# Optimization experiments

Measured on AMD Instinct MI355X. Metric: run time of the kernel, lower is better.

The kernel has to match this reference:

```python
import jax, jax.numpy as jnp
import numpy as np

EPS = 1e-4

def _conv(x, W):
    # x: [B,H,W,Cin], W: [3,3,Cin,Cout] -> SAME submanifold-style dense conv
    return jax.lax.conv_general_dilated(x, W, (1, 1), 'SAME',
                                        dimension_numbers=('NHWC', 'HWIO', 'NHWC'))

def _bn_relu(x, m, g, b):
    # BatchNormReLU over active sites only (scn semantics)
    mm = m[..., None]
    n = jnp.maximum(mm.sum(), 1.0)
    mean = (x * mm).sum((0, 1, 2)) / n
    var = (((x - mean) ** 2) * mm).sum((0, 1, 2)) / n
    y = (x - mean) * jax.lax.rsqrt(var + EPS) * g + b
    return jnp.maximum(y, 0.0) * mm

def _maxpool(x, m):
    # scn.MaxPooling(2, 3, 2): 3x3 window, stride 2, VALID; output active if any input active
    neg = jnp.where(m[..., None] > 0, x, -1e30)
    p = jax.lax.reduce_window(neg, -1e30, jax.lax.max, (1, 3, 3, 1), (1, 2, 2, 1), 'VALID')
    m2 = jax.lax.reduce_window(m, 0.0, jax.lax.max, (1, 3, 3), (1, 2, 2), 'VALID')
    return jnp.where(m2[..., None] > 0, p, 0.0), m2


def setup_inputs() -> dict:
    key = jax.random.key(0)
    ks = jax.random.split(key, 16)
    B, H, W = 2048, 23, 31
    x = jax.random.normal(ks[0], (B, H, W, 2), dtype=jnp.float32)
    mask = jax.random.randint(ks[1], (B, H, W), 0, 2, dtype=jnp.int32)
    def w(k, shape, s=0.05):
        return jax.random.normal(k, shape, dtype=jnp.float32) * s
    params = {
        'x': x, 'mask': mask,
        'W1': w(ks[2], (3, 3, 2, 16)),   'g1': jnp.ones(16),  'b1': jnp.zeros(16),
        'W2': w(ks[3], (3, 3, 16, 32)),  'g2': jnp.ones(32),  'b2': jnp.zeros(32),
        'W3': w(ks[4], (3, 3, 32, 64)),  'g3': jnp.ones(64),  'b3': jnp.zeros(64),
        'W4': w(ks[5], (3, 3, 64, 128)), 'g4': jnp.ones(128), 'b4': jnp.zeros(128),
        'Wl': w(ks[6], (3, 3, 128, 4 * 256)), 'bl': jnp.zeros(4 * 256),
        'lw1': w(ks[7], (8960, 1024), 0.02), 'lb1': jnp.zeros(1024),
        'lw2': w(ks[8], (1024, 5 * 7 * 12), 0.02), 'lb2': jnp.zeros(5 * 7 * 12),
    }
    return params


def reference(x, mask, W1, g1, b1, W2, g2, b2, W3, g3, b3, W4, g4, b4,
              Wl, bl, lw1, lb1, lw2, lb2):
    m = mask.astype(x.dtype)
    xm = x * m[..., None]
    h = _bn_relu(_conv(xm, W1) * m[..., None], m, g1, b1)
    h = _bn_relu(_conv(h, W2) * m[..., None], m, g2, b2)
    h, m = _maxpool(h, m)                          # [B,11,15,32]
    h = _bn_relu(_conv(h, W3) * m[..., None], m, g3, b3)
    h = _bn_relu(_conv(h, W4) * m[..., None], m, g4, b4)
    h, m = _maxpool(h, m)                          # [B,5,7,128]
    # sparse ConvLSTM, single step, zero initial hidden/cell state
    gates = (_conv(h, Wl) + bl) * m[..., None]     # [B,5,7,1024]
    i, f, o, g_ = jnp.split(gates, 4, axis=-1)
    c = jax.nn.sigmoid(i) * jnp.tanh(g_)
    hh = jax.nn.sigmoid(o) * jnp.tanh(c) * m[..., None]  # [B,5,7,256]
    # SparseToDense gives [B,C,H,W]; flatten in (C,H,W) order like torch .view
    flat = jnp.transpose(hh, (0, 3, 1, 2)).reshape(hh.shape[0], -1)  # [B,8960]
    y = jnp.maximum(flat @ lw1 + lb1, 0.0)
    y = y @ lw2 + lb2
    return y.reshape(-1, 5, 7, 12)
```

## Files before the change

### kernel.cpp

```cpp
#include <hip/hip_runtime.h>
#include <hip/hip_bf16.h>
#include <math.h>

using bf16 = __hip_bfloat16;

typedef short s8v __attribute__((ext_vector_type(8)));
typedef float f4v __attribute__((ext_vector_type(4)));

static constexpr int  BB  = 2048;
static constexpr int  IH  = 23, IW = 31;
static constexpr int  PH  = 11, PW = 15;
static constexpr int  QH  = 5,  QW = 7;
static constexpr long NSITE1 = (long)BB * IH * IW;
static constexpr long NSITE2 = (long)BB * PH * PW;
static constexpr long NSITE3 = (long)BB * QH * QW;

static constexpr long OFF_S1 = 0,   OFF_Q1 = 64;
static constexpr long OFF_S2 = 128, OFF_Q2 = 192;
static constexpr long OFF_S3 = 256, OFF_Q3 = 320;
static constexpr long OFF_S4 = 384, OFF_Q4 = 512;
static constexpr long OFF_N1 = 640, OFF_N2 = 641;
static constexpr long OFF_SC1 = 704,  OFF_SH1 = 768;
static constexpr long OFF_SC2 = 832,  OFF_SH2 = 896;
static constexpr long OFF_SC3 = 960,  OFF_SH3 = 1024;
static constexpr long OFF_SC4 = 1088, OFF_SH4 = 1216;
static constexpr long OFF_M0 = 2048;
static constexpr long OFF_M1 = OFF_M0 + NSITE1;
static constexpr long OFF_M2 = OFF_M1 + NSITE2;
static constexpr long OFF_BF = 1871872;
static constexpr long SZ_A   = 43253760L;
static constexpr long WB2_A  = 25000000L;
static constexpr long WB3_B  = 22000000L;
static constexpr long WB4_B  = 22100000L;
static constexpr long WBL_A  = 20000000L;
static constexpr long WFC1_B = 23000000L;
static constexpr long WFC2_B = 33000000L;
static constexpr long BKT_A  = 40000000L;
static constexpr long BKT_B  = 35000000L;

__device__ __forceinline__ float b2f(bf16 v) { return __bfloat162float(v); }
__device__ __forceinline__ bf16  f2b(float v) { return __float2bfloat16(v); }
__device__ __forceinline__ float sigmoidf_(float x) {
    return __builtin_amdgcn_rcpf(1.f + __expf(-x));
}
__device__ __forceinline__ float tanhf_(float x) {
    float xc = fminf(fmaxf(x, -15.f), 15.f);
    float t = __expf(-2.f * xc);
    return (1.f - t) * __builtin_amdgcn_rcpf(1.f + t);
}

__device__ __forceinline__ void ld8(const bf16* p, float* f) {
    union { uint4 u; unsigned short s[8]; } cv;
    cv.u = *(const uint4*)p;
#pragma unroll
    for (int i = 0; i < 8; i++) f[i] = __uint_as_float(((unsigned int)cv.s[i]) << 16);
}
__device__ __forceinline__ void st8(bf16* p, const float* f) {
    union { uint4 u; bf16 h[8]; } cv;
#pragma unroll
    for (int i = 0; i < 8; i++) cv.h[i] = f2b(f[i]);
    *(uint4*)p = cv.u;
}

__global__ void cvt_w_k(const float* __restrict__ W, bf16* __restrict__ wb,
                        int CIN, int CINP, int COUT, int total) {
    int idx = blockIdx.x * 256 + threadIdx.x;
    if (idx >= total) return;
    int ci  = idx % CINP;
    int t2  = idx / CINP;
    int co  = t2 % COUT;
    int tap = t2 / COUT;
    wb[idx] = (ci < CIN) ? f2b(W[((long)(tap * CIN + ci)) * COUT + co]) : f2b(0.f);
}

__global__ void cvt_wl3_k(const float* __restrict__ Wl, bf16* __restrict__ wbl3) {
    int idx = blockIdx.x * 256 + threadIdx.x;
    if (idx >= 884736) return;
    int kidx = idx & 31;
    int n    = (idx >> 5) % 768;
    int kk   = (idx >> 5) / 768 % 4;
    int tap  = idx / (32 * 768 * 4);
    int g = n >> 8, c = n & 255;
    int col = (g == 0) ? c : (g == 1 ? 512 + c : 768 + c);
    int cin = kk * 32 + kidx;
    wbl3[idx] = f2b(Wl[((long)(tap * 128 + cin)) * 1024 + col]);
}

__global__ void cvt_fc1T8_k(const float* __restrict__ lw1, bf16* __restrict__ wfc1) {
    int t = blockIdx.x * 256 + threadIdx.x;
    if (t >= 1146880) return;
    int j   = t & 1023;
    int k8g = t >> 10;
    int hw  = k8g >> 5;
    int c8  = k8g & 31;
    float f[8];
#pragma unroll
    for (int c7 = 0; c7 < 8; c7++)
        f[c7] = lw1[((long)((c8 * 8 + c7) * 35 + hw)) * 1024 + j];
    st8(wfc1 + (long)t * 8, f);
}

__global__ void cvt_fc2T8_k(const float* __restrict__ lw2, bf16* __restrict__ whi,
                            bf16* __restrict__ wlo) {
    int t = blockIdx.x * 256 + threadIdx.x;
    if (t >= 57344) return;
    int n  = t % 448;
    int k8 = t / 448;
    union { uint4 u; bf16 h8[8]; } h, l;
#pragma unroll
    for (int ki = 0; ki < 8; ki++) {
        float v = (n < 420) ? lw2[(long)(k8 * 8 + ki) * 420 + n] : 0.f;
        bf16 hb = f2b(v);
        h.h8[ki] = hb;
        l.h8[ki] = f2b(v - b2f(hb));
    }
    *(uint4*)(whi + (long)t * 8) = h.u;
    *(uint4*)(wlo + (long)t * 8) = l.u;
}

__global__ void prep_k(const float* __restrict__ x, const int* __restrict__ mask,
                       float* __restrict__ m0, bf16* __restrict__ xm) {
    long idx = (long)blockIdx.x * 256 + threadIdx.x;
    if (idx >= NSITE1) return;
    float m = (mask[idx] != 0) ? 1.f : 0.f;
    m0[idx] = m;
    xm[idx * 2 + 0] = f2b(x[idx * 2 + 0] * m);
    xm[idx * 2 + 1] = f2b(x[idx * 2 + 1] * m);
}

__global__ void conv1_k(const bf16* __restrict__ xm, const float* __restrict__ Wt,
                        const float* __restrict__ m0, bf16* __restrict__ out,
                        float* __restrict__ bkt, float* __restrict__ cnt) {
    __shared__ float s_s[16], s_q[16], s_c;
    const int H = IH, W = IW;
    int tid = threadIdx.x;
    int L = tid & 63;
    if (tid < 16) { s_s[tid] = 0.f; s_q[tid] = 0.f; }
    if (tid == 0) s_c = 0.f;
    __syncthreads();
    long site = (long)blockIdx.x * 256 + tid;
    float acc[16];
#pragma unroll
    for (int i = 0; i < 16; i++) acc[i] = 0.f;
    float mk = 0.f;
    if (site < NSITE1) {
        mk = m0[site];
        if (mk > 0.f) {
            int w = (int)(site % W); int h = (int)((site / W) % H);
            for (int tap = 0; tap < 9; tap++) {
                int dh = tap / 3 - 1, dw = tap % 3 - 1;
                int nh = h + dh, nw = w + dw;
                if (nh < 0 || nh >= H || nw < 0 || nw >= W) continue;
                long ns = site + (long)dh * W + dw;
                float i0 = b2f(xm[ns * 2 + 0]), i1 = b2f(xm[ns * 2 + 1]);
                const float* wp = Wt + tap * 32;
#pragma unroll
                for (int co = 0; co < 16; co++) acc[co] += i0 * wp[co] + i1 * wp[16 + co];
            }
        }
        st8(out + site * 16, acc);
        st8(out + site * 16 + 8, acc + 8);
    }
#pragma unroll
    for (int i = 0; i < 16; i++) {
        float vb = (site < NSITE1) ? b2f(f2b(acc[i])) : 0.f;
        float s = vb, q2 = vb * vb;
#pragma unroll
        for (int off = 32; off > 0; off >>= 1) {
            s  += __shfl_xor(s, off);
            q2 += __shfl_xor(q2, off);
        }
        if (L == 0) { atomicAdd(&s_s[i], s); atomicAdd(&s_q[i], q2); }
    }
    {
        float c = (mk > 0.f) ? 1.f : 0.f;
#pragma unroll
        for (int off = 32; off > 0; off >>= 1) c += __shfl_xor(c, off);
        if (L == 0) atomicAdd(&s_c, c);
    }
    __syncthreads();
    int bk = blockIdx.x & 63;
    if (tid < 16) {
        atomicAdd(bkt + (long)bk * 32 + tid, s_s[tid]);
        atomicAdd(bkt + (long)bk * 32 + 16 + tid, s_q[tid]);
    }
    if (tid == 0) atomicAdd(cnt, s_c);
}

template<int CIN, int CINP, int COUT, int KK, int MT_W, int NT_W, int H, int W,
         bool ZPAD, bool BN, bool STATS, bool CNT>
__global__ void conv_mfma(const bf16* __restrict__ in, const bf16* __restrict__ wb,
                          const float* __restrict__ mask,
                          const float* __restrict__ scale, const float* __restrict__ shift,
                          bf16* __restrict__ out,
                          float* __restrict__ bkt, float* __restrict__ cnt) {
    constexpr int NT   = COUT / 16;
    constexpr int NWN  = NT / NT_W;
    constexpr int HALO = W + 1;
    constexpr int REG  = 64 + 2 * HALO;
    constexpr int SE   = CIN + 8;
    constexpr int CHPS = CIN / 8;
    __shared__ bf16 smem[(REG + 1) * SE];
    __shared__ float s_s[COUT], s_q[COUT], s_c;

    const int tid = threadIdx.x;
    const int wv = tid >> 6;
    const int L  = tid & 63;
    const int q  = (L >> 4);
    const int lm = L & 15;
    const int wn = wv % NWN;
    const int wm = wv / NWN;
    const int mt0 = wm * MT_W;
    const long base = (long)blockIdx.x * 64;
    const long nsites = (long)gridDim.x * 64;

    for (int c = tid; c < REG * CHPS; c += 256) {
        int s = c / CHPS;
        int o = c % CHPS;
        long gs = base - HALO + s;
        uint4 v = {0u, 0u, 0u, 0u};
        if (gs >= 0 && gs < nsites) {
            v = *(const uint4*)(in + gs * CIN + o * 8);
            if (BN) {
                float mk = mask[gs];
                union { uint4 u; unsigned short us[8]; } cv; cv.u = v;
                union { uint4 u; bf16 h[8]; } ov;
#pragma unroll
                for (int i = 0; i < 8; i++) {
                    float f = __uint_as_float(((unsigned int)cv.us[i]) << 16);
                    int ch = o * 8 + i;
                    float r = fmaxf(f * scale[ch] + shift[ch], 0.f);
                    ov.h[i] = f2b(mk > 0.f ? r : 0.f);
                }
                v = ov.u;
            }
        }
        *(uint4*)(smem + s * SE + o * 8) = v;
    }
    if (ZPAD) {
        uint4 z = {0u, 0u, 0u, 0u};
        for (int s = tid; s < REG; s += 256)
            *(uint4*)(smem + s * SE + CIN) = z;
        if (tid == 0)
            *(uint4*)(smem + REG * SE) = z;
    }
    if (STATS) {
        if (tid < COUT) { s_s[tid] = 0.f; s_q[tid] = 0.f; }
        if (tid == 0) s_c = 0.f;
    }
    __syncthreads();

    int hh[MT_W], ww[MT_W];
#pragma unroll
    for (int i = 0; i < MT_W; i++) {
        long s = base + (mt0 + i) * 16 + lm;
        ww[i] = (int)(s % W);
        hh[i] = (int)((s / W) % H);
    }
    const int lbase = mt0 * 16 + lm + HALO;

    f4v acc[MT_W][NT_W];
#pragma unroll
    for (int i = 0; i < MT_W; i++)
#pragma unroll
        for (int j = 0; j < NT_W; j++) acc[i][j] = (f4v){0.f, 0.f, 0.f, 0.f};

    for (int tap = 0; tap < 9; tap++) {
        const int dh = tap / 3 - 1, dw = tap % 3 - 1;
        const int dlo = dh * W + dw;
#pragma unroll
        for (int kk = 0; kk < KK; kk++) {
            s8v a[MT_W];
#pragma unroll
            for (int i = 0; i < MT_W; i++) {
                int nh = hh[i] + dh, nw = ww[i] + dw;
                bool ok = (nh >= 0) & (nh < H) & (nw < W) & (nw >= 0);
                s8v t = *(const s8v*)(smem + (lbase + i * 16 + dlo) * SE + kk * 32 + q * 8);
                a[i] = ok ? t : (s8v){0, 0, 0, 0, 0, 0, 0, 0};
            }
#pragma unroll
            for (int j = 0; j < NT_W; j++) {
                int co = (wn * NT_W + j) * 16 + lm;
                s8v b = *(const s8v*)(wb + ((long)(tap * COUT + co)) * CINP + kk * 32 + q * 8);
#pragma unroll
                for (int i = 0; i < MT_W; i++)
                    acc[i][j] = __builtin_amdgcn_mfma_f32_16x16x32_bf16(a[i], b, acc[i][j], 0, 0, 0);
            }
        }
    }

    float ls[NT_W], lq[NT_W];
#pragma unroll
    for (int j = 0; j < NT_W; j++) { ls[j] = 0.f; lq[j] = 0.f; }
    float lc = 0.f;
#pragma unroll
    for (int i = 0; i < MT_W; i++) {
#pragma unroll
        for (int r = 0; r < 4; r++) {
            long so = base + (mt0 + i) * 16 + q * 4 + r;
            float mk = mask[so];
            if (CNT) { if (wv == 0 && lm == 0) lc += (mk > 0.f) ? 1.f : 0.f; }
#pragma unroll
            for (int j = 0; j < NT_W; j++) {
                int co = (wn * NT_W + j) * 16 + lm;
                bf16 ob = f2b(mk > 0.f ? acc[i][j][r] : 0.f);
                out[so * COUT + co] = ob;
                if (STATS) { float vb = b2f(ob); ls[j] += vb; lq[j] += vb * vb; }
            }
        }
    }
    if (STATS) {
#pragma unroll
        for (int j = 0; j < NT_W; j++) {
            ls[j] += __shfl_xor(ls[j], 16);
            ls[j] += __shfl_xor(ls[j], 32);
            lq[j] += __shfl_xor(lq[j], 16);
            lq[j] += __shfl_xor(lq[j], 32);
            if (q == 0) {
                int co = (wn * NT_W + j) * 16 + lm;
                atomicAdd(&s_s[co], ls[j]);
                atomicAdd(&s_q[co], lq[j]);
            }
        }
        if (CNT) {
            lc += __shfl_xor(lc, 16);
            lc += __shfl_xor(lc, 32);
            if (wv == 0 && L == 0) atomicAdd(&s_c, lc);
        }
        __syncthreads();
        int bk = blockIdx.x & 63;
        if (tid < COUT) {
            atomicAdd(bkt + (long)bk * 2 * COUT + tid, s_s[tid]);
            atomicAdd(bkt + (long)bk * 2 * COUT + COUT + tid, s_q[tid]);
        }
        if (CNT && tid == 0) atomicAdd(cnt, s_c);
    }
}

template<int C>
__global__ void bn_param_bkt(const float* __restrict__ bkt, const float* __restrict__ count,
                             const float* __restrict__ g, const float* __restrict__ b,
                             float* __restrict__ scale, float* __restrict__ shift) {
    int c = threadIdx.x;
    if (c >= C) return;
    float s = 0.f, q2 = 0.f;
    for (int k = 0; k < 64; k++) {
        s  += bkt[(long)k * 2 * C + c];
        q2 += bkt[(long)k * 2 * C + C + c];
    }
    float n = fmaxf(count[0], 1.f);
    float mean = s / n;
    float var  = q2 / n - mean * mean;
    float sc = (1.f / sqrtf(var + 1e-4f)) * g[c];
    scale[c] = sc;
    shift[c] = b[c] - mean * sc;
}

template<int C>
__global__ void maxpool_bn(const bf16* __restrict__ in, const float* __restrict__ min_,
                           const float* __restrict__ scale, const float* __restrict__ shift,
                           bf16* __restrict__ out, float* __restrict__ mout,
                           int B, int H, int W, int OH, int OW) {
    long i8 = (long)blockIdx.x * 256 + threadIdx.x;
    long total8 = (long)B * OH * OW * C / 8;
    if (i8 >= total8) return;
    long e0 = i8 * 8;
    int c0 = (int)(e0 % C);
    long osite = e0 / C;
    int ow = (int)(osite % OW); long t2 = osite / OW; int oh = (int)(t2 % OH); long b = t2 / OH;
    float sc[8], sh[8];
#pragma unroll
    for (int i = 0; i < 8; i++) { sc[i] = scale[c0 + i]; sh[i] = shift[c0 + i]; }
    float mm = 0.f, p[8];
#pragma unroll
    for (int i = 0; i < 8; i++) p[i] = -1e30f;
    for (int kh = 0; kh < 3; kh++)
    for (int kw = 0; kw < 3; kw++) {
        int h = oh * 2 + kh, w = ow * 2 + kw;
        long is = ((long)b * H + h) * W + w;
        float mv = min_[is];
        if (mv > 0.f) {
            mm = 1.f;
            float f[8];
            ld8(in + is * C + c0, f);
#pragma unroll
            for (int i = 0; i < 8; i++) p[i] = fmaxf(p[i], f[i] * sc[i] + sh[i]);
        }
    }
    float o[8];
#pragma unroll
    for (int i = 0; i < 8; i++) o[i] = (mm > 0.f) ? fmaxf(p[i], 0.f) : 0.f;
    st8(out + e0, o);
    if (c0 == 0) mout[osite] = mm;
}

__global__ void maxpool_p2t(const bf16* __restrict__ c4, const float* __restrict__ m1,
                            const float* __restrict__ scale, const float* __restrict__ shift,
                            bf16* __restrict__ p2T8, float* __restrict__ m2h) {
    int t = blockIdx.x * 256 + threadIdx.x;
    if (t >= 1146880) return;
    int b  = t & 2047;
    int q2 = t >> 11;
    int hw = q2 % 35;
    int k8 = q2 / 35;
    int oh = hw / QW, ow = hw % QW;
    int c0 = k8 * 8;
    float sc[8], sh[8];
#pragma unroll
    for (int i = 0; i < 8; i++) { sc[i] = scale[c0 + i]; sh[i] = shift[c0 + i]; }
    float mm = 0.f, p[8];
#pragma unroll
    for (int i = 0; i < 8; i++) p[i] = -1e30f;
    for (int kh = 0; kh < 3; kh++)
    for (int kw = 0; kw < 3; kw++) {
        int h = oh * 2 + kh, w = ow * 2 + kw;
        long is = ((long)b * PH + h) * PW + w;
        float mv = m1[is];
        if (mv > 0.f) {
            mm = 1.f;
            float f[8];
            ld8(c4 + is * 128 + c0, f);
#pragma unroll
            for (int i = 0; i < 8; i++) p[i] = fmaxf(p[i], f[i] * sc[i] + sh[i]);
        }
    }
    float o[8];
#pragma unroll
    for (int i = 0; i < 8; i++) o[i] = (mm > 0.f) ? fmaxf(p[i], 0.f) : 0.f;
    st8(p2T8 + (long)t * 8, o);
    if (k8 == 0) m2h[hw * 2048 + b] = mm;
}

__global__ void __launch_bounds__(256, 3)
gates_mfma(const bf16* __restrict__ p2T8, const bf16* __restrict__ wbl3,
           const float* __restrict__ bl, const float* __restrict__ m2h,
           bf16* __restrict__ goutT8) {
    __shared__ bf16 abuf[16 * 64 * 8];
    __shared__ bf16 sm[64][136];
    const int bi = blockIdx.x;
    const int half = bi & 1;
    const int g2 = bi >> 1;
    const int hw = g2 >> 5;
    const int b0 = (g2 & 31) * 64;
    const int h = hw / QW, w = hw % QW;
    const int tid = threadIdx.x;
    const int wv = tid >> 6;
    const int L  = tid & 63;
    const int q  = L >> 4;
    const int lm = L & 15;

    f4v acc[4][2][3];
#pragma unroll
    for (int i = 0; i < 4; i++)
#pragma unroll
        for (int j = 0; j < 2; j++)
#pragma unroll
            for (int g = 0; g < 3; g++) acc[i][j][g] = (f4v){0.f, 0.f, 0.f, 0.f};

    for (int tap = 0; tap < 9; tap++) {
        const int dh = tap / 3 - 1, dw = tap % 3 - 1;
        const int nh = h + dh, nw = w + dw;
        if (nh < 0 || nh >= QH || nw < 0 || nw >= QW) continue;
        const int hwn = hw + dh * QW + dw;

        __syncthreads();
        for (int c = tid; c < 1024; c += 256) {
            int kq = c >> 6;
            int bb = c & 63;
            uint4 v = *(const uint4*)(p2T8 + (((long)(kq * 35 + hwn)) * 2048 + b0 + bb) * 8);
            *(uint4*)(abuf + (long)c * 8) = v;
        }
        __syncthreads();

#pragma unroll
        for (int kk = 0; kk < 4; kk++) {
            s8v a[4];
#pragma unroll
            for (int i = 0; i < 4; i++)
                a[i] = *(const s8v*)(abuf + (((kk * 4 + q) * 64) + i * 16 + lm) * 8);
            const bf16* slab = wbl3 + ((long)(tap * 4 + kk)) * 768 * 32 + (long)q * 8;
#pragma unroll
            for (int j = 0; j < 2; j++) {
                int cc = half * 8 + wv * 2 + j;
#pragma unroll
                for (int g = 0; g < 3; g++) {
                    int n = g * 256 + cc * 16 + lm;
                    s8v b = *(const s8v*)(slab + (long)n * 32);
#pragma unroll
                    for (int i = 0; i < 4; i++)
                        acc[i][j][g] = __builtin_amdgcn_mfma_f32_16x16x32_bf16(a[i], b, acc[i][j][g], 0, 0, 0);
                }
            }
        }
    }
#pragma unroll
    for (int j = 0; j < 2; j++) {
        int cc = half * 8 + wv * 2 + j;
        int c = cc * 16 + lm;
        int cl = (wv * 2 + j) * 16 + lm;
        float bi_ = bl[c], bo_ = bl[512 + c], bg_ = bl[768 + c];
#pragma unroll
        for (int i = 0; i < 4; i++) {
#pragma unroll
            for (int r = 0; r < 4; r++) {
                int b_in = i * 16 + q * 4 + r;
                float m = m2h[hw * 2048 + b0 + b_in];
                float val = 0.f;
                if (m > 0.f) {
                    float iv = acc[i][j][0][r] + bi_;
                    float ov = acc[i][j][1][r] + bo_;
                    float gv = acc[i][j][2][r] + bg_;
                    float ct = sigmoidf_(iv) * tanhf_(gv);
                    val = sigmoidf_(ov) * tanhf_(ct);
                }
                sm[b_in][cl] = f2b(val);
            }
        }
    }
    __syncthreads();
#pragma unroll
    for (int k = 0; k < 4; k++) {
        int e = k * 256 + tid;
        int c8l = e >> 6, b_in = e & 63;
        union { uint4 u; bf16 h8[8]; } v;
#pragma unroll
        for (int i = 0; i < 8; i++) v.h8[i] = sm[b_in][c8l * 8 + i];
        long dst = ((long)(hw * 32 + half * 16 + c8l)) * 2048 + b0 + b_in;
        *(uint4*)(goutT8 + dst * 8) = v.u;
    }
}

__global__ void fc1_mfma(const bf16* __restrict__ AT8, const bf16* __restrict__ WT8,
                         const float* __restrict__ lb1, bf16* __restrict__ y1) {
    const int tid = threadIdx.x;
    const int wv = tid >> 6;
    const int L  = tid & 63;
    const int q  = L >> 4, lm = L & 15;
    const int wm = wv >> 1, wn = wv & 1;
    const int bm = blockIdx.x & 31;
    const int bn = blockIdx.x >> 5;
    const int m0 = bm * 64 + wm * 32;
    const int n0 = bn * 64 + wn * 32;

    f4v acc[2][2];
#pragma unroll
    for (int i = 0; i < 2; i++)
#pragma unroll
        for (int j = 0; j < 2; j++) acc[i][j] = (f4v){0.f, 0.f, 0.f, 0.f};

#pragma unroll 2
    for (int k8 = 0; k8 < 1120; k8 += 4) {
        long ar = ((long)(k8 + q)) * 2048;
        long br = ((long)(k8 + q)) * 1024;
        s8v a0 = *(const s8v*)(AT8 + (ar + m0 + lm) * 8);
        s8v a1 = *(const s8v*)(AT8 + (ar + m0 + 16 + lm) * 8);
        s8v b0 = *(const s8v*)(WT8 + (br + n0 + lm) * 8);
        s8v b1 = *(const s8v*)(WT8 + (br + n0 + 16 + lm) * 8);
        acc[0][0] = __builtin_amdgcn_mfma_f32_16x16x32_bf16(a0, b0, acc[0][0], 0, 0, 0);
        acc[0][1] = __builtin_amdgcn_mfma_f32_16x16x32_bf16(a0, b1, acc[0][1], 0, 0, 0);
        acc[1][0] = __builtin_amdgcn_mfma_f32_16x16x32_bf16(a1, b0, acc[1][0], 0, 0, 0);
        acc[1][1] = __builtin_amdgcn_mfma_f32_16x16x32_bf16(a1, b1, acc[1][1], 0, 0, 0);
    }
#pragma unroll
    for (int i = 0; i < 2; i++) {
#pragma unroll
        for (int j = 0; j < 2; j++) {
            int nn = n0 + j * 16 + lm;
            float bias = lb1[nn];
#pragma unroll
            for (int r = 0; r < 4; r++) {
                int mm = m0 + i * 16 + q * 4 + r;
                y1[(long)mm * 1024 + nn] = f2b(fmaxf(acc[i][j][r] + bias, 0.f));
            }
        }
    }
}

__global__ void fc2_mfma(const bf16* __restrict__ y1, const bf16* __restrict__ whi,
                         const bf16* __restrict__ wlo, const float* __restrict__ lb2,
                         float* __restrict__ out) {
    const int tid = threadIdx.x;
    const int wv = tid >> 6;
    const int L  = tid & 63;
    const int q  = L >> 4, lm = L & 15;
    const int wm = wv >> 1, wn = wv & 1;
    const int bm = blockIdx.x % 32;
    const int bn = blockIdx.x / 32;
    const int m0 = bm * 64 + wm * 32;
    const int n0 = bn * 64 + wn * 32;

    f4v acc[2][2];
#pragma unroll
    for (int i = 0; i < 2; i++)
#pragma unroll
        for (int j = 0; j < 2; j++) acc[i][j] = (f4v){0.f, 0.f, 0.f, 0.f};

#pragma unroll 2
    for (int k8 = 0; k8 < 128; k8 += 4) {
        const bf16* arow = y1 + (long)(k8 + q) * 8;
        long br = ((long)(k8 + q)) * 448;
        s8v a0 = *(const s8v*)(arow + (long)(m0 + lm) * 1024);
        s8v a1 = *(const s8v*)(arow + (long)(m0 + 16 + lm) * 1024);
        s8v h0 = *(const s8v*)(whi + (br + n0 + lm) * 8);
        s8v h1 = *(const s8v*)(whi + (br + n0 + 16 + lm) * 8);
        s8v l0 = *(const s8v*)(wlo + (br + n0 + lm) * 8);
        s8v l1 = *(const s8v*)(wlo + (br + n0 + 16 + lm) * 8);
        acc[0][0] = __builtin_amdgcn_mfma_f32_16x16x32_bf16(a0, h0, acc[0][0], 0, 0, 0);
        acc[0][1] = __builtin_amdgcn_mfma_f32_16x16x32_bf16(a0, h1, acc[0][1], 0, 0, 0);
        acc[1][0] = __builtin_amdgcn_mfma_f32_16x16x32_bf16(a1, h0, acc[1][0], 0, 0, 0);
        acc[1][1] = __builtin_amdgcn_mfma_f32_16x16x32_bf16(a1, h1, acc[1][1], 0, 0, 0);
        acc[0][0] = __builtin_amdgcn_mfma_f32_16x16x32_bf16(a0, l0, acc[0][0], 0, 0, 0);
        acc[0][1] = __builtin_amdgcn_mfma_f32_16x16x32_bf16(a0, l1, acc[0][1], 0, 0, 0);
        acc[1][0] = __builtin_amdgcn_mfma_f32_16x16x32_bf16(a1, l0, acc[1][0], 0, 0, 0);
        acc[1][1] = __builtin_amdgcn_mfma_f32_16x16x32_bf16(a1, l1, acc[1][1], 0, 0, 0);
    }
#pragma unroll
    for (int j = 0; j < 2; j++) {
        int nn = n0 + j * 16 + lm;
        if (nn >= 420) continue;
        float bias = lb2[nn];
#pragma unroll
        for (int i = 0; i < 2; i++) {
#pragma unroll
            for (int r = 0; r < 4; r++) {
                int mm = m0 + i * 16 + q * 4 + r;
                out[(long)mm * 420 + nn] = acc[i][j][r] + bias;
            }
        }
    }
}

extern "C" void kernel_launch(void* const* d_in, const int* in_sizes, int n_in,
                              void* d_out, int out_size, void* d_ws, size_t ws_size,
                              hipStream_t stream) {
    const float* x    = (const float*)d_in[0];
    const int*   mask = (const int*)d_in[1];
    const float* W1 = (const float*)d_in[2];
    const float* g1 = (const float*)d_in[3];
    const float* b1 = (const float*)d_in[4];
    const float* W2 = (const float*)d_in[5];
    const float* g2 = (const float*)d_in[6];
    const float* b2 = (const float*)d_in[7];
    const float* W3 = (const float*)d_in[8];
    const float* g3 = (const float*)d_in[9];
    const float* b3 = (const float*)d_in[10];
    const float* W4 = (const float*)d_in[11];
    const float* g4 = (const float*)d_in[12];
    const float* b4 = (const float*)d_in[13];
    const float* Wl = (const float*)d_in[14];
    const float* bl = (const float*)d_in[15];
    const float* lw1 = (const float*)d_in[16];
    const float* lb1 = (const float*)d_in[17];
    const float* lw2 = (const float*)d_in[18];
    const float* lb2 = (const float*)d_in[19];
    float* out = (float*)d_out;

    float* ws = (float*)d_ws;
    float* m0 = ws + OFF_M0;
    float* m1 = ws + OFF_M1;
    float* m2h = ws + OFF_M2;
    bf16* bufA = (bf16*)(ws + OFF_BF);
    bf16* bufB = bufA + SZ_A;

    bf16* c1     = bufA;
    bf16* xm     = bufB;
    bf16* c2     = bufB;
    bf16* p1     = bufA;
    bf16* c3     = bufB;
    bf16* c4     = bufA;
    bf16* p2T8   = bufB;
    bf16* goutT8 = bufA;
    bf16* y1     = bufB;
    bf16* wb2    = bufA + WB2_A;
    bf16* wb3    = bufB + WB3_B;
    bf16* wb4    = bufB + WB4_B;
    bf16* wbl3   = bufA + WBL_A;
    bf16* wfc1   = bufB + WFC1_B;
    bf16* wfc2h  = bufB + WFC2_B;
    bf16* wfc2l  = wfc2h + 458752;

    float* bkt16  = (float*)(bufA + BKT_A);
    float* bkt32  = bkt16 + 2048;
    float* bkt64  = bkt32 + 4096;
    float* bkt128 = (float*)(bufB + BKT_B);

    hipMemsetAsync(ws, 0, 4096, stream);
    hipMemsetAsync(bkt16, 0, (2048 + 4096 + 8192) * 4, stream);

    prep_k<<<(int)((NSITE1 + 255) / 256), 256, 0, stream>>>(x, mask, m0, xm);
    cvt_w_k<<<(9216 + 255) / 256, 256, 0, stream>>>(W2, wb2, 16, 32, 32, 9216);

    conv1_k<<<(int)((NSITE1 + 255) / 256), 256, 0, stream>>>(xm, W1, m0, c1, bkt16, ws + OFF_N1);
    bn_param_bkt<16><<<1, 16, 0, stream>>>(bkt16, ws + OFF_N1, g1, b1, ws + OFF_SC1, ws + OFF_SH1);

    conv_mfma<16, 32, 32, 1, 2, 1, IH, IW, true, true, true, false>
        <<<(int)(NSITE1 / 64), 256, 0, stream>>>(c1, wb2, m0, ws + OFF_SC1, ws + OFF_SH1, c2,
                                                 bkt32, nullptr);
    bn_param_bkt<32><<<1, 32, 0, stream>>>(bkt32, ws + OFF_N1, g2, b2, ws + OFF_SC2, ws + OFF_SH2);

    maxpool_bn<32><<<(int)(NSITE2 * 32 / 8 / 256), 256, 0, stream>>>(c2, m0, ws + OFF_SC2, ws + OFF_SH2,
                                                                     p1, m1, BB, IH, IW, PH, PW);

    hipMemsetAsync(bkt128, 0, 16384 * 4, stream);
    cvt_w_k<<<(18432 + 255) / 256, 256, 0, stream>>>(W3, wb3, 32, 32, 64, 18432);
    cvt_w_k<<<(73728 + 255) / 256, 256, 0, stream>>>(W4, wb4, 64, 64, 128, 73728);
    cvt_fc1T8_k<<<(1146880 + 255) / 256, 256, 0, stream>>>(lw1, wfc1);
    cvt_fc2T8_k<<<(57344 + 255) / 256, 256, 0, stream>>>(lw2, wfc2h, wfc2l);

    conv_mfma<32, 32, 64, 1, 4, 1, PH, PW, false, false, true, true>
        <<<(int)(NSITE2 / 64), 256, 0, stream>>>(p1, wb3, m1, ws + OFF_SC2, ws + OFF_SH2, c3,
                                                 bkt64, ws + OFF_N2);
    bn_param_bkt<64><<<1, 64, 0, stream>>>(bkt64, ws + OFF_N2, g3, b3, ws + OFF_SC3, ws + OFF_SH3);

    conv_mfma<64, 64, 128, 2, 4, 2, PH, PW, false, true, true, false>
        <<<(int)(NSITE2 / 64), 256, 0, stream>>>(c3, wb4, m1, ws + OFF_SC3, ws + OFF_SH3, c4,
                                                 bkt128, nullptr);
    bn_param_bkt<128><<<1, 128, 0, stream>>>(bkt128, ws + OFF_N2, g4, b4, ws + OFF_SC4, ws + OFF_SH4);

    maxpool_p2t<<<(1146880 + 255) / 256, 256, 0, stream>>>(c4, m1, ws + OFF_SC4, ws + OFF_SH4, p2T8, m2h);

    cvt_wl3_k<<<(884736 + 255) / 256, 256, 0, stream>>>(Wl, wbl3);

    gates_mfma<<<2240, 256, 0, stream>>>(p2T8, wbl3, bl, m2h, goutT8);

    fc1_mfma<<<512, 256, 0, stream>>>(goutT8, wfc1, lb1, y1);

    fc2_mfma<<<224, 256, 0, stream>>>(y1, wfc2h, wfc2l, lb2, out);
}
```

Baseline: 891.6 us.

## Fold BN parameter kernels into consumers and merge weight-conversion launches

Removes the four single-block bn_param_bkt launches by having each consumer kernel (conv_mfma with BN, maxpool_bn, maxpool_p2t) reduce the 64 stat buckets into shared-memory scale/shift at block start. It also merges prep with the W2 conversion and the W3/W4/fc1/fc2 weight conversions into single multi-role kernels, and consolidates memsets. This cuts launch count and serial gaps between tiny kernels. In exchange every block redundantly sums the buckets and adds a barrier before its main work.

```diff
diff --git a/kernel.cpp b/kernel.cpp
--- a/kernel.cpp
+++ b/kernel.cpp
@@ -15,15 +15,7 @@
 static constexpr long NSITE2 = (long)BB * PH * PW;
 static constexpr long NSITE3 = (long)BB * QH * QW;
 
-static constexpr long OFF_S1 = 0,   OFF_Q1 = 64;
-static constexpr long OFF_S2 = 128, OFF_Q2 = 192;
-static constexpr long OFF_S3 = 256, OFF_Q3 = 320;
-static constexpr long OFF_S4 = 384, OFF_Q4 = 512;
 static constexpr long OFF_N1 = 640, OFF_N2 = 641;
-static constexpr long OFF_SC1 = 704,  OFF_SH1 = 768;
-static constexpr long OFF_SC2 = 832,  OFF_SH2 = 896;
-static constexpr long OFF_SC3 = 960,  OFF_SH3 = 1024;
-static constexpr long OFF_SC4 = 1088, OFF_SH4 = 1216;
 static constexpr long OFF_M0 = 2048;
 static constexpr long OFF_M1 = OFF_M0 + NSITE1;
 static constexpr long OFF_M2 = OFF_M1 + NSITE2;
@@ -36,7 +28,7 @@
 static constexpr long WFC1_B = 23000000L;
 static constexpr long WFC2_B = 33000000L;
 static constexpr long BKT_A  = 40000000L;
-static constexpr long BKT_B  = 35000000L;
+static constexpr long BKT_B  = 34000000L;
 
 __device__ __forceinline__ float b2f(bf16 v) { return __bfloat162float(v); }
 __device__ __forceinline__ bf16  f2b(float v) { return __float2bfloat16(v); }
@@ -62,9 +54,8 @@
     *(uint4*)p = cv.u;
 }
 
-__global__ void cvt_w_k(const float* __restrict__ W, bf16* __restrict__ wb,
-                        int CIN, int CINP, int COUT, int total) {
-    int idx = blockIdx.x * 256 + threadIdx.x;
+__device__ __forceinline__ void cvt_w_body(const float* __restrict__ W, bf16* __restrict__ wb,
+                                           int CIN, int CINP, int COUT, int total, int idx) {
     if (idx >= total) return;
     int ci  = idx % CINP;
     int t2  = idx / CINP;
@@ -73,59 +64,57 @@
     wb[idx] = (ci < CIN) ? f2b(W[((long)(tap * CIN + ci)) * COUT + co]) : f2b(0.f);
 }
 
-__global__ void cvt_wl3_k(const float* __restrict__ Wl, bf16* __restrict__ wbl3) {
-    int idx = blockIdx.x * 256 + threadIdx.x;
-    if (idx >= 884736) return;
-    int kidx = idx & 31;
-    int n    = (idx >> 5) % 768;
-    int kk   = (idx >> 5) / 768 % 4;
-    int tap  = idx / (32 * 768 * 4);
-    int g = n >> 8, c = n & 255;
-    int col = (g == 0) ? c : (g == 1 ? 512 + c : 768 + c);
-    int cin = kk * 32 + kidx;
-    wbl3[idx] = f2b(Wl[((long)(tap * 128 + cin)) * 1024 + col]);
-}
-
-__global__ void cvt_fc1T8_k(const float* __restrict__ lw1, bf16* __restrict__ wfc1) {
-    int t = blockIdx.x * 256 + threadIdx.x;
-    if (t >= 1146880) return;
-    int j   = t & 1023;
-    int k8g = t >> 10;
-    int hw  = k8g >> 5;
-    int c8  = k8g & 31;
-    float f[8];
-#pragma unroll
-    for (int c7 = 0; c7 < 8; c7++)
-        f[c7] = lw1[((long)((c8 * 8 + c7) * 35 + hw)) * 1024 + j];
-    st8(wfc1 + (long)t * 8, f);
-}
-
-__global__ void cvt_fc2T8_k(const float* __restrict__ lw2, bf16* __restrict__ whi,
-                            bf16* __restrict__ wlo) {
-    int t = blockIdx.x * 256 + threadIdx.x;
-    if (t >= 57344) return;
-    int n  = t % 448;
-    int k8 = t / 448;
-    union { uint4 u; bf16 h8[8]; } h, l;
-#pragma unroll
-    for (int ki = 0; ki < 8; ki++) {
-        float v = (n < 420) ? lw2[(long)(k8 * 8 + ki) * 420 + n] : 0.f;
-        bf16 hb = f2b(v);
-        h.h8[ki] = hb;
-        l.h8[ki] = f2b(v - b2f(hb));
-    }
-    *(uint4*)(whi + (long)t * 8) = h.u;
-    *(uint4*)(wlo + (long)t * 8) = l.u;
-}
-
-__global__ void prep_k(const float* __restrict__ x, const int* __restrict__ mask,
-                       float* __restrict__ m0, bf16* __restrict__ xm) {
-    long idx = (long)blockIdx.x * 256 + threadIdx.x;
-    if (idx >= NSITE1) return;
-    float m = (mask[idx] != 0) ? 1.f : 0.f;
-    m0[idx] = m;
-    xm[idx * 2 + 0] = f2b(x[idx * 2 + 0] * m);
-    xm[idx * 2 + 1] = f2b(x[idx * 2 + 1] * m);
+__global__ void prep_cvtw2_k(const float* __restrict__ x, const int* __restrict__ mask,
+                             float* __restrict__ m0, bf16* __restrict__ xm,
+                             const float* __restrict__ W2, bf16* __restrict__ wb2) {
+    int bid = blockIdx.x, tid = threadIdx.x;
+    if (bid < 5704) {
+        long idx = (long)bid * 256 + tid;
+        float m = (mask[idx] != 0) ? 1.f : 0.f;
+        m0[idx] = m;
+        xm[idx * 2 + 0] = f2b(x[idx * 2 + 0] * m);
+        xm[idx * 2 + 1] = f2b(x[idx * 2 + 1] * m);
+    } else {
+        cvt_w_body(W2, wb2, 16, 32, 32, 9216, (bid - 5704) * 256 + tid);
+    }
+}
+
+__global__ void cvt_all_k(const float* __restrict__ W3, const float* __restrict__ W4,
+                          const float* __restrict__ lw1, const float* __restrict__ lw2,
+                          bf16* __restrict__ wb3, bf16* __restrict__ wb4,
+                          bf16* __restrict__ wfc1, bf16* __restrict__ whi,
+                          bf16* __restrict__ wlo) {
+    int bid = blockIdx.x, tid = threadIdx.x;
+    if (bid < 72) {
+        cvt_w_body(W3, wb3, 32, 32, 64, 18432, bid * 256 + tid);
+    } else if (bid < 360) {
+        cvt_w_body(W4, wb4, 64, 64, 128, 73728, (bid - 72) * 256 + tid);
+    } else if (bid < 4840) {
+        int t = (bid - 360) * 256 + tid;
+        int j   = t & 1023;
+        int k8g = t >> 10;
+        int hw  = k8g >> 5;
+        int c8  = k8g & 31;
+        float f[8];
+#pragma unroll
+        for (int c7 = 0; c7 < 8; c7++)
+            f[c7] = lw1[((long)((c8 * 8 + c7) * 35 + hw)) * 1024 + j];
+        st8(wfc1 + (long)t * 8, f);
+    } else {
+        int t = (bid - 4840) * 256 + tid;
+        int n  = t % 448;
+        int k8 = t / 448;
+        union { uint4 u; bf16 h8[8]; } h, l;
+#pragma unroll
+        for (int ki = 0; ki < 8; ki++) {
+            float v = (n < 420) ? lw2[(long)(k8 * 8 + ki) * 420 + n] : 0.f;
+            bf16 hb = f2b(v);
+            h.h8[ki] = hb;
+            l.h8[ki] = f2b(v - b2f(hb));
+        }
+        *(uint4*)(whi + (long)t * 8) = h.u;
+        *(uint4*)(wlo + (long)t * 8) = l.u;
+    }
 }
 
 __global__ void conv1_k(const bf16* __restrict__ xm, const float* __restrict__ Wt,
@@ -191,9 +180,10 @@
          bool ZPAD, bool BN, bool STATS, bool CNT>
 __global__ void conv_mfma(const bf16* __restrict__ in, const bf16* __restrict__ wb,
                           const float* __restrict__ mask,
-                          const float* __restrict__ scale, const float* __restrict__ shift,
+                          const float* __restrict__ bktIn, const float* __restrict__ cntIn,
+                          const float* __restrict__ gIn, const float* __restrict__ bIn,
                           bf16* __restrict__ out,
-                          float* __restrict__ bkt, float* __restrict__ cnt) {
+                          float* __restrict__ bktOut, float* __restrict__ cntOut) {
     constexpr int NT   = COUT / 16;
     constexpr int NWN  = NT / NT_W;
     constexpr int HALO = W + 1;
@@ -202,6 +192,7 @@
     constexpr int CHPS = CIN / 8;
     __shared__ bf16 smem[(REG + 1) * SE];
     __shared__ float s_s[COUT], s_q[COUT], s_c;
+    __shared__ float s_sc[CIN], s_sh[CIN];
 
     const int tid = threadIdx.x;
     const int wv = tid >> 6;
@@ -213,6 +204,23 @@
     const int mt0 = wm * MT_W;
     const long base = (long)blockIdx.x * 64;
     const long nsites = (long)gridDim.x * 64;
+
+    if (BN) {
+        if (tid < CIN) {
+            float s = 0.f, q2 = 0.f;
+            for (int k = 0; k < 64; k++) {
+                s  += bktIn[(long)k * 2 * CIN + tid];
+                q2 += bktIn[(long)k * 2 * CIN + CIN + tid];
+            }
+            float n = fmaxf(cntIn[0], 1.f);
+            float mean = s / n;
+            float var  = q2 / n - mean * mean;
+            float scv = (1.f / sqrtf(var + 1e-4f)) * gIn[tid];
+            s_sc[tid] = scv;
+            s_sh[tid] = bIn[tid] - mean * scv;
+        }
+        __syncthreads();
+    }
 
     for (int c = tid; c < REG * CHPS; c += 256) {
         int s = c / CHPS;
@@ -229,7 +237,7 @@
                 for (int i = 0; i < 8; i++) {
                     float f = __uint_as_float(((unsigned int)cv.us[i]) << 16);
                     int ch = o * 8 + i;
-                    float r = fmaxf(f * scale[ch] + shift[ch], 0.f);
+                    float r = fmaxf(f * s_sc[ch] + s_sh[ch], 0.f);
                     ov.h[i] = f2b(mk > 0.f ? r : 0.f);
                 }
                 v = ov.u;
@@ -330,38 +338,36 @@
         __syncthreads();
         int bk = blockIdx.x & 63;
         if (tid < COUT) {
-            atomicAdd(bkt + (long)bk * 2 * COUT + tid, s_s[tid]);
-            atomicAdd(bkt + (long)bk * 2 * COUT + COUT + tid, s_q[tid]);
-        }
-        if (CNT && tid == 0) atomicAdd(cnt, s_c);
-    }
-}
-
-template<int C>
-__global__ void bn_param_bkt(const float* __restrict__ bkt, const float* __restrict__ count,
-                             const float* __restrict__ g, const float* __restrict__ b,
-                             float* __restrict__ scale, float* __restrict__ shift) {
-    int c = threadIdx.x;
-    if (c >= C) return;
-    float s = 0.f, q2 = 0.f;
-    for (int k = 0; k < 64; k++) {
-        s  += bkt[(long)k * 2 * C + c];
-        q2 += bkt[(long)k * 2 * C + C + c];
-    }
-    float n = fmaxf(count[0], 1.f);
-    float mean = s / n;
-    float var  = q2 / n - mean * mean;
-    float sc = (1.f / sqrtf(var + 1e-4f)) * g[c];
-    scale[c] = sc;
-    shift[c] = b[c] - mean * sc;
+            atomicAdd(bktOut + (long)bk * 2 * COUT + tid, s_s[tid]);
+            atomicAdd(bktOut + (long)bk * 2 * COUT + COUT + tid, s_q[tid]);
+        }
+        if (CNT && tid == 0) atomicAdd(cntOut, s_c);
+    }
 }
 
 template<int C>
 __global__ void maxpool_bn(const bf16* __restrict__ in, const float* __restrict__ min_,
-                           const float* __restrict__ scale, const float* __restrict__ shift,
+                           const float* __restrict__ bkt, const float* __restrict__ cnt,
+                           const float* __restrict__ g, const float* __restrict__ b_,
                            bf16* __restrict__ out, float* __restrict__ mout,
                            int B, int H, int W, int OH, int OW) {
-    long i8 = (long)blockIdx.x * 256 + threadIdx.x;
+    __shared__ float ssc[C], ssh[C];
+    int tid = threadIdx.x;
+    if (tid < C) {
+        float s = 0.f, q2 = 0.f;
+        for (int k = 0; k < 64; k++) {
+            s  += bkt[(long)k * 2 * C + tid];
+            q2 += bkt[(long)k * 2 * C + C + tid];
+        }
+        float n = fmaxf(cnt[0], 1.f);
+        float mean = s / n;
+        float var  = q2 / n - mean * mean;
+        float scv = (1.f / sqrtf(var + 1e-4f)) * g[tid];
+        ssc[tid] = scv;
+        ssh[tid] = b_[tid] - mean * scv;
+    }
+    __syncthreads();
+    long i8 = (long)blockIdx.x * 256 + tid;
     long total8 = (long)B * OH * OW * C / 8;
     if (i8 >= total8) return;
     long e0 = i8 * 8;
@@ -370,7 +376,7 @@
     int ow = (int)(osite % OW); long t2 = osite / OW; int oh = (int)(t2 % OH); long b = t2 / OH;
     float sc[8], sh[8];
 #pragma unroll
-    for (int i = 0; i < 8; i++) { sc[i] = scale[c0 + i]; sh[i] = shift[c0 + i]; }
+    for (int i = 0; i < 8; i++) { sc[i] = ssc[c0 + i]; sh[i] = ssh[c0 + i]; }
     float mm = 0.f, p[8];
 #pragma unroll
     for (int i = 0; i < 8; i++) p[i] = -1e30f;
@@ -395,19 +401,36 @@
 }
 
 __global__ void maxpool_p2t(const bf16* __restrict__ c4, const float* __restrict__ m1,
-                            const float* __restrict__ scale, const float* __restrict__ shift,
+                            const float* __restrict__ bkt, const float* __restrict__ cnt,
+                            const float* __restrict__ g, const float* __restrict__ b_,
                             bf16* __restrict__ p2T8, float* __restrict__ m2h) {
-    int t = blockIdx.x * 256 + threadIdx.x;
+    __shared__ float ssc[128], ssh[128];
+    int tid = threadIdx.x;
+    if (tid < 128) {
+        float s = 0.f, q2 = 0.f;
+        for (int k = 0; k < 64; k++) {
+            s  += bkt[(long)k * 256 + tid];
+            q2 += bkt[(long)k * 256 + 128 + tid];
+        }
+        float n = fmaxf(cnt[0], 1.f);
+        float mean = s / n;
+        float var  = q2 / n - mean * mean;
+        float scv = (1.f / sqrtf(var + 1e-4f)) * g[tid];
+        ssc[tid] = scv;
+        ssh[tid] = b_[tid] - mean * scv;
+    }
+    __syncthreads();
+    int t = blockIdx.x * 256 + tid;
     if (t >= 1146880) return;
     int b  = t & 2047;
-    int q2 = t >> 11;
-    int hw = q2 % 35;
-    int k8 = q2 / 35;
+    int q2i = t >> 11;
+    int hw = q2i % 35;
+    int k8 = q2i / 35;
     int oh = hw / QW, ow = hw % QW;
     int c0 = k8 * 8;
     float sc[8], sh[8];
 #pragma unroll
-    for (int i = 0; i < 8; i++) { sc[i] = scale[c0 + i]; sh[i] = shift[c0 + i]; }
+    for (int i = 0; i < 8; i++) { sc[i] = ssc[c0 + i]; sh[i] = ssh[c0 + i]; }
     float mm = 0.f, p[8];
 #pragma unroll
     for (int i = 0; i < 8; i++) p[i] = -1e30f;
@@ -429,6 +452,19 @@
     for (int i = 0; i < 8; i++) o[i] = (mm > 0.f) ? fmaxf(p[i], 0.f) : 0.f;
     st8(p2T8 + (long)t * 8, o);
     if (k8 == 0) m2h[hw * 2048 + b] = mm;
+}
+
+__global__ void cvt_wl3_k(const float* __restrict__ Wl, bf16* __restrict__ wbl3) {
+    int idx = blockIdx.x * 256 + threadIdx.x;
+    if (idx >= 884736) return;
+    int kidx = idx & 31;
+    int n    = (idx >> 5) % 768;
+    int kk   = (idx >> 5) / 768 % 4;
+    int tap  = idx / (32 * 768 * 4);
+    int g = n >> 8, c = n & 255;
+    int col = (g == 0) ? c : (g == 1 ? 512 + c : 768 + c);
+    int cin = kk * 32 + kidx;
+    wbl3[idx] = f2b(Wl[((long)(tap * 128 + cin)) * 1024 + col]);
 }
 
 __global__ void __launch_bounds__(256, 3)
@@ -681,43 +717,38 @@
 
     float* bkt16  = (float*)(bufA + BKT_A);
     float* bkt32  = bkt16 + 2048;
-    float* bkt64  = bkt32 + 4096;
-    float* bkt128 = (float*)(bufB + BKT_B);
+    float* bkt64  = (float*)(bufB + BKT_B);
+    float* bkt128 = bkt64 + 8192;
 
     hipMemsetAsync(ws, 0, 4096, stream);
-    hipMemsetAsync(bkt16, 0, (2048 + 4096 + 8192) * 4, stream);
-
-    prep_k<<<(int)((NSITE1 + 255) / 256), 256, 0, stream>>>(x, mask, m0, xm);
-    cvt_w_k<<<(9216 + 255) / 256, 256, 0, stream>>>(W2, wb2, 16, 32, 32, 9216);
-
-    conv1_k<<<(int)((NSITE1 + 255) / 256), 256, 0, stream>>>(xm, W1, m0, c1, bkt16, ws + OFF_N1);
-    bn_param_bkt<16><<<1, 16, 0, stream>>>(bkt16, ws + OFF_N1, g1, b1, ws + OFF_SC1, ws + OFF_SH1);
+    hipMemsetAsync(bkt16, 0, (2048 + 4096) * 4, stream);
+
+    prep_cvtw2_k<<<5740, 256, 0, stream>>>(x, mask, m0, xm, W2, wb2);
+
+    conv1_k<<<5704, 256, 0, stream>>>(xm, W1, m0, c1, bkt16, ws + OFF_N1);
 
     conv_mfma<16, 32, 32, 1, 2, 1, IH, IW, true, true, true, false>
-        <<<(int)(NSITE1 / 64), 256, 0, stream>>>(c1, wb2, m0, ws + OFF_SC1, ws + OFF_SH1, c2,
-                                                 bkt32, nullptr);
-    bn_param_bkt<32><<<1, 32, 0, stream>>>(bkt32, ws + OFF_N1, g2, b2, ws + OFF_SC2, ws + OFF_SH2);
-
-    maxpool_bn<32><<<(int)(NSITE2 * 32 / 8 / 256), 256, 0, stream>>>(c2, m0, ws + OFF_SC2, ws + OFF_SH2,
-                                                                     p1, m1, BB, IH, IW, PH, PW);
-
-    hipMemsetAsync(bkt128, 0, 16384 * 4, stream);
-    cvt_w_k<<<(18432 + 255) / 256, 256, 0, stream>>>(W3, wb3, 32, 32, 64, 18432);
-    cvt_w_k<<<(73728 + 255) / 256, 256, 0, stream>>>(W4, wb4, 64, 64, 128, 73728);
-    cvt_fc1T8_k<<<(1146880 + 255) / 256, 256, 0, stream>>>(lw1, wfc1);
-    cvt_fc2T8_k<<<(57344 + 255) / 256, 256, 0, stream>>>(lw2, wfc2h, wfc2l);
+        <<<(int)(NSITE1 / 64), 256, 0, stream>>>(c1, wb2, m0,
+                                                 bkt16, ws + OFF_N1, g1, b1,
+                                                 c2, bkt32, nullptr);
+
+    maxpool_bn<32><<<(int)(NSITE2 * 32 / 8 / 256), 256, 0, stream>>>(
+        c2, m0, bkt32, ws + OFF_N1, g2, b2, p1, m1, BB, IH, IW, PH, PW);
+
+    hipMemsetAsync(bkt64, 0, (8192 + 16384) * 4, stream);
+    cvt_all_k<<<5064, 256, 0, stream>>>(W3, W4, lw1, lw2, wb3, wb4, wfc1, wfc2h, wfc2l);
 
     conv_mfma<32, 32, 64, 1, 4, 1, PH, PW, false, false, true, true>
-        <<<(int)(NSITE2 / 64), 256, 0, stream>>>(p1, wb3, m1, ws + OFF_SC2, ws + OFF_SH2, c3,
-                                                 bkt64, ws + OFF_N2);
-    bn_param_bkt<64><<<1, 64, 0, stream>>>(bkt64, ws + OFF_N2, g3, b3, ws + OFF_SC3, ws + OFF_SH3);
+        <<<(int)(NSITE2 / 64), 256, 0, stream>>>(p1, wb3, m1,
+                                                 nullptr, nullptr, nullptr, nullptr,
+                                                 c3, bkt64, ws + OFF_N2);
 
     conv_mfma<64, 64, 128, 2, 4, 2, PH, PW, false, true, true, false>
-        <<<(int)(NSITE2 / 64), 256, 0, stream>>>(c3, wb4, m1, ws + OFF_SC3, ws + OFF_SH3, c4,
-                                                 bkt128, nullptr);
-    bn_param_bkt<128><<<1, 128, 0, stream>>>(bkt128, ws + OFF_N2, g4, b4, ws + OFF_SC4, ws + OFF_SH4);
-
-    maxpool_p2t<<<(1146880 + 255) / 256, 256, 0, stream>>>(c4, m1, ws + OFF_SC4, ws + OFF_SH4, p2T8, m2h);
+        <<<(int)(NSITE2 / 64), 256, 0, stream>>>(c3, wb4, m1,
+                                                 bkt64, ws + OFF_N2, g3, b3,
+                                                 c4, bkt128, nullptr);
+
+    maxpool_p2t<<<4480, 256, 0, stream>>>(c4, m1, bkt128, ws + OFF_N2, g4, b4, p2T8, m2h);
 
     cvt_wl3_k<<<(884736 + 255) / 256, 256, 0, stream>>>(Wl, wbl3);
 
```

New measurement: 895.2 us. Within noise of the previous version (+0.4%).
